# Optimization experiments

Hardware: AMD Instinct MI355X
Metric: run time of the kernel (lower is better)

## Reference

```python
import jax, jax.numpy as jnp
import numpy as np
from jax import lax

DIM = 512
HEADS = 8
SPLIT = 7  # split_size; idx=0 -> H_sp=H, W_sp=SPLIT


def setup_inputs() -> dict:
    key = jax.random.key(0)
    k1, k2 = jax.random.split(key, 2)
    B, H, W = 16, 56, 56
    qkv = jax.random.normal(k1, (3, B, H * W, DIM), dtype=jnp.float32)
    conv_w = jax.random.normal(k2, (DIM, 1, 3, 3), dtype=jnp.float32) * 0.05  # depthwise 3x3
    conv_b = jnp.zeros((DIM,), dtype=jnp.float32)
    return {"qkv": qkv, "conv_w": conv_w, "conv_b": conv_b, "H": H, "W": W}


def _lepe_attn(qkv, conv_w, conv_b, H, W):
    q, k, v = qkv[0], qkv[1], qkv[2]
    B, L, C = q.shape
    hd = C // HEADS
    scale = hd ** -0.5
    H_sp, W_sp = H, SPLIT  # idx == 0 (horizontal stripes)
    S = H_sp * W_sp
    nWh, nWw = H // H_sp, W // W_sp

    def to_win_heads(x):
        # [B, L, C] -> [B*nW, heads, S, hd]
        x = x.reshape(B, nWh, H_sp, nWw, W_sp, C)
        x = x.transpose(0, 1, 3, 2, 4, 5).reshape(-1, S, HEADS, hd)
        return x.transpose(0, 2, 1, 3)

    qw = to_win_heads(q)
    kw = to_win_heads(k)

    # v as per-window images [B*nW, C, H_sp, W_sp] for depthwise-conv LePE
    vimg = v.reshape(B, nWh, H_sp, nWw, W_sp, C)
    vimg = vimg.transpose(0, 1, 3, 5, 2, 4).reshape(-1, C, H_sp, W_sp)
    lepe = lax.conv_general_dilated(
        vimg, conv_w, window_strides=(1, 1), padding=[(1, 1), (1, 1)],
        dimension_numbers=("NCHW", "OIHW", "NCHW"), feature_group_count=C,
    ) + conv_b[None, :, None, None]
    lepe = lepe.reshape(-1, HEADS, hd, S).transpose(0, 1, 3, 2)  # [B*nW, heads, S, hd]
    vw = vimg.reshape(-1, HEADS, hd, S).transpose(0, 1, 3, 2)

    attn = jnp.einsum("whsd,whtd->whst", qw * scale, kw)
    attn = jax.nn.softmax(attn, axis=-1)
    out = jnp.einsum("whst,whtd->whsd", attn, vw) + lepe

    # windows -> image: [B*nW, heads, S, hd] -> [B, L, C]
    out = out.transpose(0, 2, 1, 3).reshape(-1, S, C)
    out = out.reshape(B, nWh, nWw, H_sp, W_sp, C)
    out = out.transpose(0, 1, 3, 2, 4, 5).reshape(B, L, C)
    return out


def reference(qkv, conv_w, conv_b, H, W):
    return _lepe_attn(qkv, conv_w, conv_b, H, W)
```

## Files before the change

### kernel.cpp

```cpp
#include <hip/hip_runtime.h>

#define B_    16
#define HIMG  56
#define WIMG  56
#define L_    3136
#define C_    512
#define NH_   8
#define HD_   64
#define S_    392
#define NCH   7
#define NQT   25

typedef short short4v __attribute__((ext_vector_type(4)));
typedef short short8  __attribute__((ext_vector_type(8)));
typedef float f32x4   __attribute__((ext_vector_type(4)));

__device__ __forceinline__ short f2bf(float f) {
    union { float f; unsigned int i; } x; x.f = f;
    unsigned int i = x.i;
    i += 0x7fffu + ((i >> 16) & 1u);
    return (short)(i >> 16);
}
__device__ __forceinline__ int l_of(int s, int ww) {
    int h = s / 7;
    int wp = s - h * 7;
    return h * WIMG + ww * 7 + wp;
}

__global__ __launch_bounds__(256) void lepe_kernel(
    const float* __restrict__ vp, const float* __restrict__ cw,
    const float* __restrict__ cb, float* __restrict__ out)
{
    __shared__ __align__(16) float sW[9 * 516];

    for (int i = threadIdx.x; i < 1152; i += 256) {
        f32x4 v = *(const f32x4*)(cw + i * 4);
#pragma unroll
        for (int j = 0; j < 4; ++j) {
            int e = 4 * i + j;
            int c = e / 9;
            int k = e - 9 * c;
            sW[k * 516 + c] = v[j];
        }
    }
    __syncthreads();

    int g    = blockIdx.x * 256 + threadIdx.x;
    int c0   = (g & 127) * 4;
    int rest = g >> 7;
    int l    = rest % L_;
    int h    = l / WIMG;
    int wim  = l - h * WIMG;
    int wsp  = wim % 7;

    f32x4 acc = *(const f32x4*)(cb + c0);
    const long long base = (long long)rest * C_ + c0;
#pragma unroll
    for (int dh = -1; dh <= 1; ++dh) {
        int hh = h + dh;
        if (hh < 0 || hh >= HIMG) continue;
#pragma unroll
        for (int dw = -1; dw <= 1; ++dw) {
            int wp2 = wsp + dw;
            if (wp2 < 0 || wp2 >= 7) continue;
            f32x4 vv = *(const f32x4*)(vp + base + (long long)(dh * WIMG + dw) * C_);
            int k = (dh + 1) * 3 + (dw + 1);
            f32x4 wv = *(const f32x4*)&sW[k * 516 + c0];
#pragma unroll
            for (int i = 0; i < 4; ++i) acc[i] += vv[i] * wv[i];
        }
    }
    *(f32x4*)(out + base) = acc;
}

__global__ __launch_bounds__(512) void attn_kernel(
    const float* __restrict__ qkv, float* __restrict__ out)
{
    const int head = blockIdx.x;
    const int win  = blockIdx.y;
    const int b    = win >> 3;
    const int ww   = win & 7;

    const int tid  = threadIdx.x;
    const int wave = tid >> 6;
    const int lane = tid & 63;
    const int ln   = lane & 15;
    const int quad = lane >> 4;

    const float* kp = qkv + (long long)B_ * L_ * C_;
    const float* vp = qkv + 2LL * (long long)B_ * L_ * C_;

    __shared__ __align__(16) short sAll[66112];
    short* sK = sAll;
    short* sV = sAll + 28224;
    short* sP = sAll + 56896 + wave * 1152;

    const int st_r = tid >> 4;
    const int st_c = (tid & 15) * 4;

    const long long kvbase = (long long)b * L_ * C_ + head * HD_;

#pragma unroll
    for (int p = 0; p < 13; ++p) {
        int t = p * 32 + st_r;
        if (t < S_) {
            f32x4 kv = *(const f32x4*)(kp + kvbase + (long long)l_of(t, ww) * C_ + st_c);
            short4v ks;
#pragma unroll
            for (int j = 0; j < 4; ++j) ks[j] = f2bf(kv[j]);
            *(short4v*)&sK[t * 72 + st_c] = ks;
        }
    }
#pragma unroll
    for (int p = 0; p < 14; ++p) {
        int t = p * 32 + st_r;
        f32x4 vv = {0.f, 0.f, 0.f, 0.f};
        if (t < S_)
            vv = *(const f32x4*)(vp + kvbase + (long long)l_of(t, ww) * C_ + st_c);
        int tb = t & ~63, tl = t & 63;
#pragma unroll
        for (int j = 0; j < 4; ++j) {
            int d  = st_c + j;
            int sw = ((d >> 3) & 7) << 3;
            sV[d * 448 + tb + (tl ^ sw)] = f2bf(vv[j]);
        }
    }
    __syncthreads();

    const float SCL = 0.125f * 1.44269504088896340736f;

    for (int qt = wave; qt < NQT; qt += 8) {
        const int qrow0 = qt * 16;
        int qs = qrow0 + ln; if (qs > S_ - 1) qs = S_ - 1;
        const long long qoff = (long long)b * L_ * C_ + (long long)l_of(qs, ww) * C_ + head * HD_ + quad * 8;
        short8 aq0, aq1;
        {
            f32x4 x0 = *(const f32x4*)(qkv + qoff);
            f32x4 x1 = *(const f32x4*)(qkv + qoff + 4);
            f32x4 x2 = *(const f32x4*)(qkv + qoff + 32);
            f32x4 x3 = *(const f32x4*)(qkv + qoff + 36);
#pragma unroll
            for (int j = 0; j < 4; ++j) {
                aq0[j] = f2bf(x0[j]); aq0[4 + j] = f2bf(x1[j]);
                aq1[j] = f2bf(x2[j]); aq1[4 + j] = f2bf(x3[j]);
            }
        }

        f32x4 Oa[4];
        float mrun[4], lrun[4];
#pragma unroll
        for (int dt = 0; dt < 4; ++dt) { Oa[dt][0]=0.f; Oa[dt][1]=0.f; Oa[dt][2]=0.f; Oa[dt][3]=0.f; }
#pragma unroll
        for (int r = 0; r < 4; ++r) { mrun[r] = -1e30f; lrun[r] = 0.f; }

        for (int ch = 0; ch < NCH; ++ch) {
            const int t0 = ch * 64;
            f32x4 sc[4];
#pragma unroll
            for (int nt = 0; nt < 4; ++nt) {
                int row = t0 + nt * 16 + ln;
                if (row > S_ - 1) row = S_ - 1;
                f32x4 acc = {0.f, 0.f, 0.f, 0.f};
                short8 bk0 = *(const short8*)&sK[row * 72 + quad * 8];
                short8 bk1 = *(const short8*)&sK[row * 72 + 32 + quad * 8];
                acc = __builtin_amdgcn_mfma_f32_16x16x32_bf16(aq0, bk0, acc, 0, 0, 0);
                acc = __builtin_amdgcn_mfma_f32_16x16x32_bf16(aq1, bk1, acc, 0, 0, 0);
                sc[nt] = acc;
            }
#pragma unroll
            for (int nt = 0; nt < 4; ++nt) {
                int t = t0 + nt * 16 + ln;
#pragma unroll
                for (int r = 0; r < 4; ++r) {
                    float v = sc[nt][r] * SCL;
                    sc[nt][r] = (t < S_) ? v : -1e30f;
                }
            }
#pragma unroll
            for (int r = 0; r < 4; ++r) {
                float mx = fmaxf(fmaxf(sc[0][r], sc[1][r]), fmaxf(sc[2][r], sc[3][r]));
                mx = fmaxf(mx, __shfl_xor(mx, 1));
                mx = fmaxf(mx, __shfl_xor(mx, 2));
                mx = fmaxf(mx, __shfl_xor(mx, 4));
                mx = fmaxf(mx, __shfl_xor(mx, 8));
                float mnew  = fmaxf(mrun[r], mx);
                float alpha = exp2f(mrun[r] - mnew);
                float p0 = exp2f(sc[0][r] - mnew);
                float p1 = exp2f(sc[1][r] - mnew);
                float p2 = exp2f(sc[2][r] - mnew);
                float p3 = exp2f(sc[3][r] - mnew);
                float rs = (p0 + p1) + (p2 + p3);
                rs += __shfl_xor(rs, 1);
                rs += __shfl_xor(rs, 2);
                rs += __shfl_xor(rs, 4);
                rs += __shfl_xor(rs, 8);
                lrun[r] = lrun[r] * alpha + rs;
                mrun[r] = mnew;
#pragma unroll
                for (int dt = 0; dt < 4; ++dt) Oa[dt][r] *= alpha;
                int row = quad * 4 + r;
                sP[row * 72 +  0 + ln] = f2bf(p0);
                sP[row * 72 + 16 + ln] = f2bf(p1);
                sP[row * 72 + 32 + ln] = f2bf(p2);
                sP[row * 72 + 48 + ln] = f2bf(p3);
            }
#pragma unroll
            for (int kc = 0; kc < 2; ++kc) {
                short8 ap = *(const short8*)&sP[ln * 72 + kc * 32 + quad * 8];
#pragma unroll
                for (int dt = 0; dt < 4; ++dt) {
                    int d     = dt * 16 + ln;
                    int colsw = (kc * 32 + quad * 8) ^ (((d >> 3) & 7) << 3);
                    short8 bv = *(const short8*)&sV[d * 448 + t0 + colsw];
                    Oa[dt] = __builtin_amdgcn_mfma_f32_16x16x32_bf16(ap, bv, Oa[dt], 0, 0, 0);
                }
            }
        }

        float inv[4];
#pragma unroll
        for (int r = 0; r < 4; ++r) inv[r] = 1.0f / lrun[r];
#pragma unroll
        for (int r = 0; r < 4; ++r) {
            int row = qrow0 + quad * 4 + r;
            if (row < S_) {
                float* op = out + (long long)b * L_ * C_ + (long long)l_of(row, ww) * C_ + head * HD_ + ln;
#pragma unroll
                for (int dt = 0; dt < 4; ++dt)
                    op[dt * 16] += Oa[dt][r] * inv[r];
            }
        }
    }
}

extern "C" void kernel_launch(void* const* d_in, const int* in_sizes, int n_in,
                              void* d_out, int out_size, void* d_ws, size_t ws_size,
                              hipStream_t stream) {
    (void)in_sizes; (void)n_in; (void)d_ws; (void)ws_size; (void)out_size;
    const float* qkv = (const float*)d_in[0];
    const float* cw  = (const float*)d_in[1];
    const float* cb  = (const float*)d_in[2];
    float* out = (float*)d_out;
    const float* vp = qkv + 2LL * (long long)B_ * L_ * C_;

    lepe_kernel<<<dim3((B_ * L_ * (C_ / 4)) / 256), dim3(256), 0, stream>>>(vp, cw, cb, out);
    attn_kernel<<<dim3(NH_, B_ * 8), dim3(512), 0, stream>>>(qkv, out);
}
```

Measured before the change: 669.9 us.

## Switch attention to 32x32 MFMA with register-resident P and lazy rescaling

Rewrites the attention inner loop around 32x32x16 bf16 MFMA, computing S^T so probabilities stay in registers. They are packed with v_cvt_pk_bf16_f32 and exchanged across half-waves with shuffles instead of round-tripping through an LDS P buffer. It also skips the online-softmax rescale unless the max grows by more than a threshold, and writes the output with vectorized f32x4 read-modify-write. The V LDS swizzle changes to suit the new access pattern. Query tiles become 32 rows (13 tiles), so each of the 8 waves handles at most 2 tiles, and the imbalance between waves could limit the gain.

```diff
diff --git a/kernel.cpp b/kernel.cpp
--- a/kernel.cpp
+++ b/kernel.cpp
@@ -8,12 +8,13 @@
 #define NH_   8
 #define HD_   64
 #define S_    392
-#define NCH   7
-#define NQT   25
+#define NKT   13
+#define NQT   13
 
 typedef short short4v __attribute__((ext_vector_type(4)));
 typedef short short8  __attribute__((ext_vector_type(8)));
 typedef float f32x4   __attribute__((ext_vector_type(4)));
+typedef float f32x16  __attribute__((ext_vector_type(16)));
 
 __device__ __forceinline__ short f2bf(float f) {
     union { float f; unsigned int i; } x; x.f = f;
@@ -84,16 +85,15 @@
     const int tid  = threadIdx.x;
     const int wave = tid >> 6;
     const int lane = tid & 63;
-    const int ln   = lane & 15;
-    const int quad = lane >> 4;
+    const int l31  = lane & 31;
+    const int hi   = lane >> 5;
 
     const float* kp = qkv + (long long)B_ * L_ * C_;
     const float* vp = qkv + 2LL * (long long)B_ * L_ * C_;
 
-    __shared__ __align__(16) short sAll[66112];
+    __shared__ __align__(16) short sAll[56896];
     short* sK = sAll;
     short* sV = sAll + 28224;
-    short* sP = sAll + 56896 + wave * 1152;
 
     const int st_r = tid >> 4;
     const int st_c = (tid & 15) * 4;
@@ -117,12 +117,11 @@
         f32x4 vv = {0.f, 0.f, 0.f, 0.f};
         if (t < S_)
             vv = *(const f32x4*)(vp + kvbase + (long long)l_of(t, ww) * C_ + st_c);
-        int tb = t & ~63, tl = t & 63;
 #pragma unroll
         for (int j = 0; j < 4; ++j) {
             int d  = st_c + j;
-            int sw = ((d >> 3) & 7) << 3;
-            sV[d * 448 + tb + (tl ^ sw)] = f2bf(vv[j]);
+            int sw = ((d >> 3) & 3) << 4;
+            sV[d * 448 + (t ^ sw)] = f2bf(vv[j]);
         }
     }
     __syncthreads();
@@ -130,104 +129,120 @@
     const float SCL = 0.125f * 1.44269504088896340736f;
 
     for (int qt = wave; qt < NQT; qt += 8) {
-        const int qrow0 = qt * 16;
-        int qs = qrow0 + ln; if (qs > S_ - 1) qs = S_ - 1;
-        const long long qoff = (long long)b * L_ * C_ + (long long)l_of(qs, ww) * C_ + head * HD_ + quad * 8;
-        short8 aq0, aq1;
-        {
-            f32x4 x0 = *(const f32x4*)(qkv + qoff);
-            f32x4 x1 = *(const f32x4*)(qkv + qoff + 4);
-            f32x4 x2 = *(const f32x4*)(qkv + qoff + 32);
-            f32x4 x3 = *(const f32x4*)(qkv + qoff + 36);
-#pragma unroll
-            for (int j = 0; j < 4; ++j) {
-                aq0[j] = f2bf(x0[j]); aq0[4 + j] = f2bf(x1[j]);
-                aq1[j] = f2bf(x2[j]); aq1[4 + j] = f2bf(x3[j]);
-            }
-        }
-
-        f32x4 Oa[4];
-        float mrun[4], lrun[4];
-#pragma unroll
-        for (int dt = 0; dt < 4; ++dt) { Oa[dt][0]=0.f; Oa[dt][1]=0.f; Oa[dt][2]=0.f; Oa[dt][3]=0.f; }
-#pragma unroll
-        for (int r = 0; r < 4; ++r) { mrun[r] = -1e30f; lrun[r] = 0.f; }
-
-        for (int ch = 0; ch < NCH; ++ch) {
-            const int t0 = ch * 64;
-            f32x4 sc[4];
-#pragma unroll
-            for (int nt = 0; nt < 4; ++nt) {
-                int row = t0 + nt * 16 + ln;
-                if (row > S_ - 1) row = S_ - 1;
-                f32x4 acc = {0.f, 0.f, 0.f, 0.f};
-                short8 bk0 = *(const short8*)&sK[row * 72 + quad * 8];
-                short8 bk1 = *(const short8*)&sK[row * 72 + 32 + quad * 8];
-                acc = __builtin_amdgcn_mfma_f32_16x16x32_bf16(aq0, bk0, acc, 0, 0, 0);
-                acc = __builtin_amdgcn_mfma_f32_16x16x32_bf16(aq1, bk1, acc, 0, 0, 0);
-                sc[nt] = acc;
-            }
-#pragma unroll
-            for (int nt = 0; nt < 4; ++nt) {
-                int t = t0 + nt * 16 + ln;
-#pragma unroll
-                for (int r = 0; r < 4; ++r) {
-                    float v = sc[nt][r] * SCL;
-                    sc[nt][r] = (t < S_) ? v : -1e30f;
+        const int qrow0 = qt * 32;
+        int qs = qrow0 + l31; if (qs > S_ - 1) qs = S_ - 1;
+        const float* qp = qkv + (long long)b * L_ * C_
+                        + (long long)l_of(qs, ww) * C_ + head * HD_ + hi * 8;
+        short8 bq[4];
+#pragma unroll
+        for (int kk = 0; kk < 4; ++kk) {
+            f32x4 x0 = *(const f32x4*)(qp + kk * 16);
+            f32x4 x1 = *(const f32x4*)(qp + kk * 16 + 4);
+            short8 t;
+#pragma unroll
+            for (int j = 0; j < 4; ++j) { t[j] = f2bf(x0[j]); t[4 + j] = f2bf(x1[j]); }
+            bq[kk] = t;
+        }
+
+        f32x16 Oa0, Oa1;
+#pragma unroll
+        for (int r = 0; r < 16; ++r) { Oa0[r] = 0.f; Oa1[r] = 0.f; }
+        float mrun = -1e30f, lrun = 0.f;
+
+        for (int ch = 0; ch < NKT; ++ch) {
+            const int kt0 = ch * 32;
+            int krow = kt0 + l31; if (krow > S_ - 1) krow = S_ - 1;
+            const short* kr = &sK[krow * 72 + hi * 8];
+
+            f32x16 acc;
+#pragma unroll
+            for (int r = 0; r < 16; ++r) acc[r] = 0.f;
+#pragma unroll
+            for (int kk = 0; kk < 4; ++kk) {
+                short8 ak = *(const short8*)(kr + kk * 16);
+                acc = __builtin_amdgcn_mfma_f32_32x32x16_bf16(ak, bq[kk], acc, 0, 0, 0);
+            }
+            float pm = -1e30f;
+#pragma unroll
+            for (int r = 0; r < 16; ++r) {
+                int key = kt0 + (r & 3) + 8 * (r >> 2) + 4 * hi;
+                float v = acc[r] * SCL;
+                v = (key < S_) ? v : -1e30f;
+                acc[r] = v;
+                pm = fmaxf(pm, v);
+            }
+            pm = fmaxf(pm, __shfl_xor(pm, 32));
+            if (__any(pm > mrun + 8.f)) {
+                float mnew  = fmaxf(mrun, pm);
+                float alpha = exp2f(mrun - mnew);
+#pragma unroll
+                for (int r = 0; r < 16; ++r) { Oa0[r] *= alpha; Oa1[r] *= alpha; }
+                lrun *= alpha;
+                mrun = mnew;
+            }
+            float rs = 0.f;
+#pragma unroll
+            for (int r = 0; r < 16; ++r) {
+                float p = exp2f(acc[r] - mrun);
+                acc[r] = p;
+                rs += p;
+            }
+            rs += __shfl_xor(rs, 32);
+            lrun += rs;
+            unsigned int u[8];
+#pragma unroll
+            for (int a = 0; a < 4; ++a)
+#pragma unroll
+                for (int h = 0; h < 2; ++h) {
+                    unsigned int r_;
+                    asm("v_cvt_pk_bf16_f32 %0, %1, %2"
+                        : "=v"(r_) : "v"(acc[4 * a + 2 * h]), "v"(acc[4 * a + 2 * h + 1]));
+                    u[a * 2 + h] = r_;
                 }
-            }
-#pragma unroll
-            for (int r = 0; r < 4; ++r) {
-                float mx = fmaxf(fmaxf(sc[0][r], sc[1][r]), fmaxf(sc[2][r], sc[3][r]));
-                mx = fmaxf(mx, __shfl_xor(mx, 1));
-                mx = fmaxf(mx, __shfl_xor(mx, 2));
-                mx = fmaxf(mx, __shfl_xor(mx, 4));
-                mx = fmaxf(mx, __shfl_xor(mx, 8));
-                float mnew  = fmaxf(mrun[r], mx);
-                float alpha = exp2f(mrun[r] - mnew);
-                float p0 = exp2f(sc[0][r] - mnew);
-                float p1 = exp2f(sc[1][r] - mnew);
-                float p2 = exp2f(sc[2][r] - mnew);
-                float p3 = exp2f(sc[3][r] - mnew);
-                float rs = (p0 + p1) + (p2 + p3);
-                rs += __shfl_xor(rs, 1);
-                rs += __shfl_xor(rs, 2);
-                rs += __shfl_xor(rs, 4);
-                rs += __shfl_xor(rs, 8);
-                lrun[r] = lrun[r] * alpha + rs;
-                mrun[r] = mnew;
-#pragma unroll
-                for (int dt = 0; dt < 4; ++dt) Oa[dt][r] *= alpha;
-                int row = quad * 4 + r;
-                sP[row * 72 +  0 + ln] = f2bf(p0);
-                sP[row * 72 + 16 + ln] = f2bf(p1);
-                sP[row * 72 + 32 + ln] = f2bf(p2);
-                sP[row * 72 + 48 + ln] = f2bf(p3);
-            }
-#pragma unroll
-            for (int kc = 0; kc < 2; ++kc) {
-                short8 ap = *(const short8*)&sP[ln * 72 + kc * 32 + quad * 8];
-#pragma unroll
-                for (int dt = 0; dt < 4; ++dt) {
-                    int d     = dt * 16 + ln;
-                    int colsw = (kc * 32 + quad * 8) ^ (((d >> 3) & 7) << 3);
-                    short8 bv = *(const short8*)&sV[d * 448 + t0 + colsw];
-                    Oa[dt] = __builtin_amdgcn_mfma_f32_16x16x32_bf16(ap, bv, Oa[dt], 0, 0, 0);
+#pragma unroll
+            for (int kkp = 0; kkp < 2; ++kkp) {
+                unsigned int sA0 = (unsigned int)__shfl_xor((int)u[4 * kkp + 0], 32);
+                unsigned int sA1 = (unsigned int)__shfl_xor((int)u[4 * kkp + 1], 32);
+                unsigned int sB0 = (unsigned int)__shfl_xor((int)u[4 * kkp + 2], 32);
+                unsigned int sB1 = (unsigned int)__shfl_xor((int)u[4 * kkp + 3], 32);
+                union { unsigned int w[4]; short8 s; } pb;
+                pb.w[0] = hi ? sB0 : u[4 * kkp + 0];
+                pb.w[1] = hi ? sB1 : u[4 * kkp + 1];
+                pb.w[2] = hi ? u[4 * kkp + 2] : sA0;
+                pb.w[3] = hi ? u[4 * kkp + 3] : sA1;
+                const int Tb = kt0 + kkp * 16 + hi * 8;
+                {
+                    int d = l31;
+                    short8 av = *(const short8*)&sV[d * 448 + (Tb ^ (((d >> 3) & 3) << 4))];
+                    Oa0 = __builtin_amdgcn_mfma_f32_32x32x16_bf16(av, pb.s, Oa0, 0, 0, 0);
                 }
-            }
-        }
-
-        float inv[4];
-#pragma unroll
-        for (int r = 0; r < 4; ++r) inv[r] = 1.0f / lrun[r];
-#pragma unroll
-        for (int r = 0; r < 4; ++r) {
-            int row = qrow0 + quad * 4 + r;
-            if (row < S_) {
-                float* op = out + (long long)b * L_ * C_ + (long long)l_of(row, ww) * C_ + head * HD_ + ln;
-#pragma unroll
-                for (int dt = 0; dt < 4; ++dt)
-                    op[dt * 16] += Oa[dt][r] * inv[r];
+                {
+                    int d = 32 + l31;
+                    short8 av = *(const short8*)&sV[d * 448 + (Tb ^ (((d >> 3) & 3) << 4))];
+                    Oa1 = __builtin_amdgcn_mfma_f32_32x32x16_bf16(av, pb.s, Oa1, 0, 0, 0);
+                }
+            }
+        }
+
+        if (qrow0 + l31 < S_) {
+            float inv = 1.0f / lrun;
+            float* op = out + (long long)b * L_ * C_
+                      + (long long)l_of(qrow0 + l31, ww) * C_ + head * HD_;
+#pragma unroll
+            for (int g = 0; g < 4; ++g) {
+                float* p4 = op + g * 8 + hi * 4;
+                f32x4 t = *(f32x4*)p4;
+#pragma unroll
+                for (int j = 0; j < 4; ++j) t[j] += Oa0[4 * g + j] * inv;
+                *(f32x4*)p4 = t;
+            }
+#pragma unroll
+            for (int g = 0; g < 4; ++g) {
+                float* p4 = op + 32 + g * 8 + hi * 4;
+                f32x4 t = *(f32x4*)p4;
+#pragma unroll
+                for (int j = 0; j < 4; ++j) t[j] += Oa1[4 * g + j] * inv;
+                *(f32x4*)p4 = t;
             }
         }
     }
```

New measurement: 588.3 us. -12.2%, faster.
